# Performance work log

Hardware: AMD Instinct MI355X
Metric: run time of the kernel (lower is better)

The kernel has to match this reference:

```python
import jax, jax.numpy as jnp
import numpy as np

N_NODES = 100000
N_EDGES = 3200000
NFEAT, NHID, NCLASS = 512, 256, 64


def spmm(rows, cols, vals, x):
    # out[i] = sum_{e: rows[e]==i} vals[e] * x[cols[e]]
    msgs = vals[:, None] * x[cols]  # [E, F]
    return jax.ops.segment_sum(msgs, rows, num_segments=N_NODES)


def setup_inputs() -> dict:
    key = jax.random.key(0)
    ks = jax.random.split(key, 12)
    x = jax.random.normal(ks[0], (N_NODES, NFEAT), dtype=jnp.float32)
    adj_rows = jax.random.randint(ks[1], (N_EDGES,), 0, N_NODES, dtype=jnp.int32)
    adj_cols = jax.random.randint(ks[2], (N_EDGES,), 0, N_NODES, dtype=jnp.int32)
    adj_vals = jax.random.uniform(ks[3], (N_EDGES,), dtype=jnp.float32)
    # xavier-uniform style init for linear weights
    def xavier(k, fan_in, fan_out):
        a = np.sqrt(6.0 / (fan_in + fan_out)).astype(np.float32)
        return jax.random.uniform(k, (fan_in, fan_out), minval=-a, maxval=a, dtype=jnp.float32)
    W1 = xavier(ks[4], NFEAT, NHID)
    b1 = jnp.zeros((NHID,), dtype=jnp.float32)
    W2 = xavier(ks[5], NHID, NCLASS)
    b2 = jnp.zeros((NCLASS,), dtype=jnp.float32)
    Wres = xavier(ks[6], NHID, NCLASS)
    bres = jnp.zeros((NCLASS,), dtype=jnp.float32)
    return {"x": x, "adj_rows": adj_rows, "adj_cols": adj_cols, "adj_vals": adj_vals,
            "W1": W1, "b1": b1, "W2": W2, "b2": b2, "Wres": Wres, "bres": bres}


def reference(x, adj_rows, adj_cols, adj_vals, W1, b1, W2, b2, Wres, bres):
    # layer 1: spmm -> linear (res_con True but last_hidden is None -> no residual)
    h = spmm(adj_rows, adj_cols, adj_vals, x)          # [N, NFEAT]
    h = h @ W1 + b1                                    # [N, NHID]
    last_hidden = h
    # dropout in eval mode: identity
    # layer 2: spmm -> linear -> relu + res(last_hidden) since NHID != NCLASS
    o = spmm(adj_rows, adj_cols, adj_vals, h)          # [N, NHID]
    o = o @ W2 + b2                                    # [N, NCLASS]
    o = jax.nn.relu(o) + (last_hidden @ Wres + bres)   # [N, NCLASS]
    return o
```

## Files before the change

kernel.cpp:

```cpp
#include <hip/hip_runtime.h>

#define N_NODES 100000
#define N_EDGES 3200000
#define NFEAT 512
#define NHID 256
#define NCLASS 64
#define FCAT 128

#define RPB 32
#define NB 3125
#define CHUNK 16384
#define NCH 196

#define ISC20 (1.0f / 1048576.0f)
#define ISC14 (1.0f / 16384.0f)
#define ISC10 (1.0f / 1024.0f)

typedef __attribute__((ext_vector_type(8))) short short8;
typedef __attribute__((ext_vector_type(4))) float f32x4;

static __device__ __forceinline__ unsigned short f2bf(float f) {
    unsigned u = __float_as_uint(f);
    unsigned r = (u + 0x7FFF + ((u >> 16) & 1)) >> 16;
    return (unsigned short)r;
}
static __device__ __forceinline__ short8 cvt8(float4 x, float4 y) {
    short8 r;
    r[0] = (short)f2bf(x.x); r[1] = (short)f2bf(x.y);
    r[2] = (short)f2bf(x.z); r[3] = (short)f2bf(x.w);
    r[4] = (short)f2bf(y.x); r[5] = (short)f2bf(y.y);
    r[6] = (short)f2bf(y.z); r[7] = (short)f2bf(y.w);
    return r;
}
__device__ __forceinline__ void gload_lds16(const unsigned short* g, unsigned short* l) {
    __builtin_amdgcn_global_load_lds(
        (const __attribute__((address_space(1))) unsigned int*)g,
        (__attribute__((address_space(3))) unsigned int*)l, 16, 0, 0);
}
static __device__ __forceinline__ int f2q10(float a) {
    return __float2int_rn(fminf(fmaxf(a, -15.98f), 15.98f) * 1024.f);
}

__global__ __launch_bounds__(256) void k_fusedA(const float* __restrict__ W1,
                                                const float* __restrict__ W2,
                                                const float* __restrict__ Wres,
                                                const float* __restrict__ b1,
                                                const float* __restrict__ bres,
                                                unsigned short* __restrict__ WT,
                                                float* __restrict__ c2,
                                                float* __restrict__ cr,
                                                const int* __restrict__ rows,
                                                int* __restrict__ HT) {
    __shared__ int h[NB];
    int tid = threadIdx.x;
    if (blockIdx.x < 256) {
        int k = blockIdx.x * 2 + (tid >> 7);
        int j = tid & 127;
        const float* wb = (j < NCLASS) ? W2 : Wres;
        int jj = j & (NCLASS - 1);
        const float* w1row = W1 + (size_t)k * NHID;
        float acc = 0.f;
        for (int m = 0; m < NHID; ++m)
            acc += w1row[m] * wb[(size_t)m * NCLASS + jj];
        WT[(size_t)j * NFEAT + k] = f2bf(acc);
        return;
    }
    if (blockIdx.x == 256) {
        if (tid < 128) {
            int j = tid;
            const float* wb = (j < NCLASS) ? W2 : Wres;
            int jj = j & (NCLASS - 1);
            float acc = 0.f;
            for (int m = 0; m < NHID; ++m)
                acc += b1[m] * wb[(size_t)m * NCLASS + jj];
            if (j < NCLASS) c2[jj] = acc;
            else            cr[jj] = acc + bres[jj];
        }
        return;
    }
    int c = blockIdx.x - 257;
    for (int i = tid; i < NB; i += 256) h[i] = 0;
    __syncthreads();
    int e0 = c * CHUNK;
    int eend = e0 + CHUNK; if (eend > N_EDGES) eend = N_EDGES;
    int i = e0 + tid;
    for (; i + 7 * 256 < eend; i += 8 * 256) {
        int r[8];
#pragma unroll
        for (int u = 0; u < 8; ++u) r[u] = rows[i + u * 256];
#pragma unroll
        for (int u = 0; u < 8; ++u) atomicAdd(&h[r[u] >> 5], 1);
    }
    for (; i < eend; i += 256)
        atomicAdd(&h[rows[i] >> 5], 1);
    __syncthreads();
    for (int k = tid; k < NB; k += 256)
        HT[(size_t)k * NCH + c] = h[k];
}

__global__ void k_scan_chunks(const int* __restrict__ HT, int* __restrict__ OFS,
                              int* __restrict__ T) {
    int b = blockIdx.x;
    int lane = threadIdx.x;
    const int* hb = HT + (size_t)b * NCH;
    int run = 0;
    for (int c0 = 0; c0 < NCH; c0 += 64) {
        int idx = c0 + lane;
        int v = (idx < NCH) ? hb[idx] : 0;
        int inc = v;
#pragma unroll
        for (int d = 1; d < 64; d <<= 1) {
            int t = __shfl_up(inc, d);
            if (lane >= d) inc += t;
        }
        if (idx < NCH) OFS[(size_t)idx * NB + b] = run + inc - v;
        run += __shfl(inc, 63);
    }
    if (lane == 0) T[b] = run;
}

__global__ void k_scan_base(const int* __restrict__ T, int* __restrict__ base) {
    int lane = threadIdx.x;
    int run = 0;
    for (int c0 = 0; c0 < NB; c0 += 64) {
        int idx = c0 + lane;
        int v = (idx < NB) ? T[idx] : 0;
        int inc = v;
#pragma unroll
        for (int d = 1; d < 64; d <<= 1) {
            int t = __shfl_up(inc, d);
            if (lane >= d) inc += t;
        }
        if (idx < NB) base[idx] = run + inc - v;
        run += __shfl(inc, 63);
    }
    if (lane == 0) base[NB] = run;
}

#define GBK 64
__global__ __launch_bounds__(256) void k_fusedB(const int* __restrict__ rows,
                                                const int* __restrict__ cols,
                                                const float* __restrict__ vals,
                                                const int* __restrict__ OFS,
                                                const int* __restrict__ base,
                                                unsigned* __restrict__ stage,
                                                const float* __restrict__ X,
                                                const unsigned short* __restrict__ WT,
                                                unsigned* __restrict__ A2) {
    __shared__ __align__(16) char smem[32768];
    int tid = threadIdx.x;

    if (blockIdx.x < NCH) {
        int* cur = (int*)smem;
        int c = blockIdx.x;
        for (int i = tid; i < NB; i += 256)
            cur[i] = base[i] + OFS[(size_t)c * NB + i];
        __syncthreads();
        int e0 = c * CHUNK;
        int eend = e0 + CHUNK; if (eend > N_EDGES) eend = N_EDGES;
        int i = e0 + tid;
        for (; i + 7 * 256 < eend; i += 8 * 256) {
            int r[8], cc[8]; float v[8];
#pragma unroll
            for (int u = 0; u < 8; ++u) r[u] = rows[i + u * 256];
#pragma unroll
            for (int u = 0; u < 8; ++u) cc[u] = cols[i + u * 256];
#pragma unroll
            for (int u = 0; u < 8; ++u) v[u] = vals[i + u * 256];
            int p[8];
#pragma unroll
            for (int u = 0; u < 8; ++u) p[u] = atomicAdd(&cur[r[u] >> 5], 1);
#pragma unroll
            for (int u = 0; u < 8; ++u) {
                unsigned v10 = min(1023u, (unsigned)__float2int_rn(v[u] * 1024.f));
                stage[p[u]] = (((unsigned)(r[u] & 31)) << 27) |
                              (((unsigned)cc[u]) << 10) | v10;
            }
        }
        for (; i < eend; i += 256) {
            int r = rows[i];
            int p = atomicAdd(&cur[r >> 5], 1);
            unsigned v10 = min(1023u, (unsigned)__float2int_rn(vals[i] * 1024.f));
            stage[p] = (((unsigned)(r & 31)) << 27) | (((unsigned)cols[i]) << 10) | v10;
        }
        return;
    }

    unsigned short* Bs = (unsigned short*)smem;
    int g = blockIdx.x - NCH;
    int lane = tid & 63, w = tid >> 6;
    int lr = lane & 15, ls = lane >> 4;
    int row = g * 64 + w * 16 + lr;
    if (row >= N_NODES) row = N_NODES - 1;
    const float* pA = X + (size_t)row * NFEAT;

#define STAGE(buf, k0)                                                         \
    {                                                                          \
        _Pragma("unroll")                                                      \
        for (int q = 0; q < 4; ++q) {                                          \
            int sidx = q * 256 + tid;                                          \
            int n = sidx >> 3, c8 = sidx & 7;                                  \
            const unsigned short* src =                                        \
                WT + (size_t)n * NFEAT + (k0) + ((c8 ^ (n & 7)) << 3);         \
            unsigned short* dst =                                              \
                Bs + (size_t)(buf) * FCAT * GBK + (size_t)(q * 256 + w * 64) * 8; \
            gload_lds16(src, dst);                                             \
        }                                                                      \
    }

    f32x4 acc[8] = {};
    STAGE(0, 0);
    __syncthreads();
    int cur = 0;

#pragma unroll
    for (int t = 0; t < 8; ++t) {
        const int k0 = t * GBK;
        float4 a00 = *(const float4*)(pA + k0 + ls * 8);
        float4 a01 = *(const float4*)(pA + k0 + ls * 8 + 4);
        float4 a10 = *(const float4*)(pA + k0 + 32 + ls * 8);
        float4 a11 = *(const float4*)(pA + k0 + 32 + ls * 8 + 4);
        if (t < 7) STAGE(cur ^ 1, k0 + GBK);

        short8 af0 = cvt8(a00, a01);
        short8 af1 = cvt8(a10, a11);
        const unsigned short* bb = Bs + (size_t)cur * FCAT * GBK;
#pragma unroll
        for (int nf = 0; nf < 8; ++nf) {
            int n = nf * 16 + lr;
            int p0 = ls ^ (n & 7);
            int p1 = (4 + ls) ^ (n & 7);
            short8 b0 = *(const short8*)(bb + (size_t)n * 64 + p0 * 8);
            short8 b1 = *(const short8*)(bb + (size_t)n * 64 + p1 * 8);
            acc[nf] = __builtin_amdgcn_mfma_f32_16x16x32_bf16(af0, b0, acc[nf], 0, 0, 0);
            acc[nf] = __builtin_amdgcn_mfma_f32_16x16x32_bf16(af1, b1, acc[nf], 0, 0, 0);
        }
        __syncthreads();
        cur ^= 1;
    }
#undef STAGE

#pragma unroll
    for (int j = 0; j < 4; ++j) {
        int gr = g * 64 + w * 16 + ls * 4 + j;
        if (gr < N_NODES) {
#pragma unroll
            for (int nf = 0; nf < 4; ++nf) {
                int il = f2q10(acc[nf][j]);
                int ih = f2q10(acc[nf + 4][j]);
                A2[(size_t)gr * 64 + nf * 16 + lr] =
                    ((unsigned)il & 0xffffu) | ((unsigned)ih << 16);
            }
        }
    }
}

__global__ __launch_bounds__(256) void k_spmm1(const unsigned* __restrict__ A2,
                                               const int* __restrict__ base,
                                               const unsigned* __restrict__ stage,
                                               unsigned short* __restrict__ S1a,
                                               float* __restrict__ S1r) {
    __shared__ int acc[RPB][FCAT];
    int b = blockIdx.x, tid = threadIdx.x;
    int wv = tid >> 6, lane = tid & 63;
    unsigned lane4 = (unsigned)lane << 2;
    int4* az = (int4*)&acc[0][0];
    for (int i = tid; i < RPB * FCAT / 4; i += 256) az[i] = make_int4(0, 0, 0, 0);
    __syncthreads();

    const char* A2b = (const char*)A2;

    int s = base[b], e = base[b + 1];
    int per = (e - s + 3) >> 2;
    int ws = s + wv * per;
    int we = ws + per; if (we > e) we = e;
    int t = ws;
    for (; t + 16 <= we; t += 16) {
        unsigned cv[16];
#pragma unroll
        for (int u = 0; u < 16; ++u) cv[u] = stage[t + u];
        unsigned p[16];
#pragma unroll
        for (int u = 0; u < 16; ++u)
            p[u] = *(const unsigned*)(A2b + (((cv[u] & 0x07FFFC00u) >> 2) | lane4));
#pragma unroll
        for (int u = 0; u < 16; ++u) {
            int v10 = (int)(cv[u] & 0x3FFu);
            int alo = (int)(short)(p[u] & 0xffffu);
            int ahi = (int)p[u] >> 16;
            int rl = (int)(cv[u] >> 27);
            atomicAdd(&acc[rl][lane],      __mul24(alo, v10));
            atomicAdd(&acc[rl][lane + 64], __mul24(ahi, v10));
        }
    }
    for (; t < we; ++t) {
        unsigned cv = stage[t];
        unsigned p = *(const unsigned*)(A2b + (((cv & 0x07FFFC00u) >> 2) | lane4));
        int v10 = (int)(cv & 0x3FFu);
        int alo = (int)(short)(p & 0xffffu);
        int ahi = (int)p >> 16;
        int rl = (int)(cv >> 27);
        atomicAdd(&acc[rl][lane],      __mul24(alo, v10));
        atomicAdd(&acc[rl][lane + 64], __mul24(ahi, v10));
    }
    __syncthreads();

#pragma unroll
    for (int rr = 0; rr < 8; ++rr) {
        int r = wv * 8 + rr;
        int node = b * RPB + r;
        int sf = (acc[r][lane] + 2048) >> 12;
        sf = max(-32760, min(32760, sf));
        S1a[(size_t)node * 64 + (lane & 31) * 2 + (lane >> 5)] = (unsigned short)sf;
        S1r[(size_t)node * 64 + lane] = (float)acc[r][lane + 64] * ISC20;
    }
}

__global__ __launch_bounds__(256) void k_spmm2_out(const unsigned* __restrict__ S1aP,
                                                   const float* __restrict__ S1r,
                                                   const int* __restrict__ base,
                                                   const unsigned* __restrict__ stage,
                                                   const float* __restrict__ c2,
                                                   const float* __restrict__ cr,
                                                   const float* __restrict__ b2,
                                                   float* __restrict__ out) {
    __shared__ int acc[RPB][NCLASS];
    __shared__ int rs[RPB];
    int b = blockIdx.x, tid = threadIdx.x;
    int wv = tid >> 6, lane = tid & 63;
    int h = lane >> 5, l5 = lane & 31;
    unsigned l54 = (unsigned)l5 << 2;
    int4* az = (int4*)&acc[0][0];
    for (int i = tid; i < RPB * NCLASS / 4; i += 256) az[i] = make_int4(0, 0, 0, 0);
    if (tid < RPB) rs[tid] = 0;
    __syncthreads();

    const char* Sb = (const char*)S1aP;

    int s = base[b], e = base[b + 1];
    int per = (e - s + 3) >> 2;
    int ws = s + wv * per;
    int we = ws + per; if (we > e) we = e;
    int t = ws;
    for (; t + 16 <= we; t += 16) {
        unsigned cv[8];
#pragma unroll
        for (int u = 0; u < 8; ++u) cv[u] = stage[t + u * 2 + h];
        unsigned p[8];
#pragma unroll
        for (int u = 0; u < 8; ++u)
            p[u] = *(const unsigned*)(Sb + (((cv[u] & 0x07FFFC00u) >> 3) | l54));
#pragma unroll
        for (int u = 0; u < 8; ++u) {
            int v10 = (int)(cv[u] & 0x3FFu);
            int slo = (int)(short)(p[u] & 0xffffu);
            int shi = (int)p[u] >> 16;
            int rl = (int)(cv[u] >> 27);
            atomicAdd(&acc[rl][l5],      (__mul24(slo, v10) + 8) >> 4);
            atomicAdd(&acc[rl][l5 + 32], (__mul24(shi, v10) + 8) >> 4);
            if (l5 == 0) atomicAdd(&rs[rl], v10);
        }
    }
    for (; t < we; t += 2) {
        int idx = t + h;
        bool act = idx < we;
        unsigned cv = stage[act ? idx : t];
        unsigned p = *(const unsigned*)(Sb + (((cv & 0x07FFFC00u) >> 3) | l54));
        int v10 = (int)(cv & 0x3FFu);
        int slo = (int)(short)(p & 0xffffu);
        int shi = (int)p >> 16;
        int rl = (int)(cv >> 27);
        if (act) {
            atomicAdd(&acc[rl][l5],      (__mul24(slo, v10) + 8) >> 4);
            atomicAdd(&acc[rl][l5 + 32], (__mul24(shi, v10) + 8) >> 4);
            if (l5 == 0) atomicAdd(&rs[rl], v10);
        }
    }
    __syncthreads();

#pragma unroll
    for (int rr = 0; rr < 8; ++rr) {
        int r = wv * 8 + rr;
        int node = b * RPB + r;
        float facc = (float)acc[r][lane] * ISC14;
        float rsum = (float)rs[r] * ISC10;
        float o = facc + rsum * c2[lane] + b2[lane];
        float res = S1r[(size_t)node * 64 + lane] + cr[lane];
        out[(size_t)node * 64 + lane] = fmaxf(o, 0.f) + res;
    }
}

extern "C" void kernel_launch(void* const* d_in, const int* in_sizes, int n_in,
                              void* d_out, int out_size, void* d_ws, size_t ws_size,
                              hipStream_t stream) {
    const float* x        = (const float*)d_in[0];
    const int*   adj_rows = (const int*)d_in[1];
    const int*   adj_cols = (const int*)d_in[2];
    const float* adj_vals = (const float*)d_in[3];
    const float* W1       = (const float*)d_in[4];
    const float* b1       = (const float*)d_in[5];
    const float* W2       = (const float*)d_in[6];
    const float* b2       = (const float*)d_in[7];
    const float* Wres     = (const float*)d_in[8];
    const float* bres     = (const float*)d_in[9];
    float* out = (float*)d_out;

    char* ws = (char*)d_ws;
    size_t off = 0;
    auto alloc = [&](size_t bytes) {
        size_t o = off;
        off += (bytes + 511) & ~511ULL;
        return o;
    };

    unsigned short* WT  = (unsigned short*)(ws + alloc((size_t)NFEAT * FCAT * 2));
    float* c2           = (float*)(ws + alloc(NCLASS * 4));
    float* cr           = (float*)(ws + alloc(NCLASS * 4));
    unsigned* stage     = (unsigned*)(ws + alloc((size_t)N_EDGES * 4));
    unsigned* A2        = (unsigned*)(ws + alloc((size_t)N_NODES * 64 * 4));
    unsigned* S1a       = (unsigned*)(ws + alloc((size_t)N_NODES * 32 * 4));
    char* s1r_region    = ws + alloc((size_t)N_NODES * 64 * 4);
    float* S1r          = (float*)s1r_region;
    int*   HT           = (int*)s1r_region;
    int*   OFS          = (int*)(s1r_region + (((size_t)NB * NCH * 4 + 511) & ~511ULL));
    int*   T            = (int*)(ws + alloc((size_t)NB * 4));
    int*   base         = (int*)(ws + alloc((size_t)(NB + 1) * 4));
    (void)ws_size; (void)in_sizes; (void)n_in; (void)out_size;

    k_fusedA<<<257 + NCH, 256, 0, stream>>>(W1, W2, Wres, b1, bres, WT, c2, cr,
                                            adj_rows, HT);

    k_scan_chunks<<<NB, 64, 0, stream>>>(HT, OFS, T);
    k_scan_base<<<1, 64, 0, stream>>>(T, base);

    k_fusedB<<<NCH + (N_NODES + 63) / 64, 256, 0, stream>>>(
        adj_rows, adj_cols, adj_vals, OFS, base, stage, x, WT, A2);

    k_spmm1<<<NB, 256, 0, stream>>>(A2, base, stage, (unsigned short*)S1a, S1r);

    k_spmm2_out<<<NB, 256, 0, stream>>>(S1a, S1r, base, stage, c2, cr, b2, out);
}
```

Before: 323.6 us.

## Quantize projected features to int8, halve partition chunk, split fused kernel

Projected layer-1 features (A2) are now quantized to 4-bit-fraction int8 (range ±7.94) instead of 10-bit-fraction int16. This halves the gather traffic in the first SpMM, which is the bandwidth-bound random access over edges. The edge partition chunk size is halved so twice as many blocks scatter into the staging buffer. The fused partition+GEMM kernel is split into two separate launches. The much coarser quantization risks accuracy loss and clipping of large activations, and the extra launch adds overhead.

```diff
diff --git a/kernel.cpp b/kernel.cpp
--- a/kernel.cpp
+++ b/kernel.cpp
@@ -9,10 +9,9 @@
 
 #define RPB 32
 #define NB 3125
-#define CHUNK 16384
-#define NCH 196
-
-#define ISC20 (1.0f / 1048576.0f)
+#define CHUNK 8192
+#define NCH 391
+
 #define ISC14 (1.0f / 16384.0f)
 #define ISC10 (1.0f / 1024.0f)
 
@@ -37,8 +36,8 @@
         (const __attribute__((address_space(1))) unsigned int*)g,
         (__attribute__((address_space(3))) unsigned int*)l, 16, 0, 0);
 }
-static __device__ __forceinline__ int f2q10(float a) {
-    return __float2int_rn(fminf(fmaxf(a, -15.98f), 15.98f) * 1024.f);
+static __device__ __forceinline__ int f2q4(float a) {
+    return __float2int_rn(fminf(fmaxf(a, -7.9375f), 7.9375f) * 16.f);
 }
 
 __global__ __launch_bounds__(256) void k_fusedA(const float* __restrict__ W1,
@@ -137,60 +136,56 @@
     if (lane == 0) base[NB] = run;
 }
 
+__global__ __launch_bounds__(256) void k_partition(const int* __restrict__ rows,
+                                                   const int* __restrict__ cols,
+                                                   const float* __restrict__ vals,
+                                                   const int* __restrict__ OFS,
+                                                   const int* __restrict__ base,
+                                                   unsigned* __restrict__ stage) {
+    __shared__ int cur[NB];
+    int c = blockIdx.x;
+    int tid = threadIdx.x;
+    for (int i = tid; i < NB; i += 256)
+        cur[i] = base[i] + OFS[(size_t)c * NB + i];
+    __syncthreads();
+    int e0 = c * CHUNK;
+    int eend = e0 + CHUNK; if (eend > N_EDGES) eend = N_EDGES;
+    int i = e0 + tid;
+    for (; i + 7 * 256 < eend; i += 8 * 256) {
+        int r[8], cc[8]; float v[8];
+#pragma unroll
+        for (int u = 0; u < 8; ++u) r[u] = rows[i + u * 256];
+#pragma unroll
+        for (int u = 0; u < 8; ++u) cc[u] = cols[i + u * 256];
+#pragma unroll
+        for (int u = 0; u < 8; ++u) v[u] = vals[i + u * 256];
+        int p[8];
+#pragma unroll
+        for (int u = 0; u < 8; ++u) p[u] = atomicAdd(&cur[r[u] >> 5], 1);
+#pragma unroll
+        for (int u = 0; u < 8; ++u) {
+            unsigned v10 = min(1023u, (unsigned)__float2int_rn(v[u] * 1024.f));
+            stage[p[u]] = (((unsigned)(r[u] & 31)) << 27) |
+                          (((unsigned)cc[u]) << 10) | v10;
+        }
+    }
+    for (; i < eend; i += 256) {
+        int r = rows[i];
+        int p = atomicAdd(&cur[r >> 5], 1);
+        unsigned v10 = min(1023u, (unsigned)__float2int_rn(vals[i] * 1024.f));
+        stage[p] = (((unsigned)(r & 31)) << 27) | (((unsigned)cols[i]) << 10) | v10;
+    }
+}
+
 #define GBK 64
-__global__ __launch_bounds__(256) void k_fusedB(const int* __restrict__ rows,
-                                                const int* __restrict__ cols,
-                                                const float* __restrict__ vals,
-                                                const int* __restrict__ OFS,
-                                                const int* __restrict__ base,
-                                                unsigned* __restrict__ stage,
-                                                const float* __restrict__ X,
+__global__ __launch_bounds__(256) void k_gemm_a(const float* __restrict__ X,
                                                 const unsigned short* __restrict__ WT,
-                                                unsigned* __restrict__ A2) {
-    __shared__ __align__(16) char smem[32768];
+                                                unsigned short* __restrict__ A2) {
+    __shared__ __align__(16) unsigned short Bs[2][FCAT * GBK];
     int tid = threadIdx.x;
-
-    if (blockIdx.x < NCH) {
-        int* cur = (int*)smem;
-        int c = blockIdx.x;
-        for (int i = tid; i < NB; i += 256)
-            cur[i] = base[i] + OFS[(size_t)c * NB + i];
-        __syncthreads();
-        int e0 = c * CHUNK;
-        int eend = e0 + CHUNK; if (eend > N_EDGES) eend = N_EDGES;
-        int i = e0 + tid;
-        for (; i + 7 * 256 < eend; i += 8 * 256) {
-            int r[8], cc[8]; float v[8];
-#pragma unroll
-            for (int u = 0; u < 8; ++u) r[u] = rows[i + u * 256];
-#pragma unroll
-            for (int u = 0; u < 8; ++u) cc[u] = cols[i + u * 256];
-#pragma unroll
-            for (int u = 0; u < 8; ++u) v[u] = vals[i + u * 256];
-            int p[8];
-#pragma unroll
-            for (int u = 0; u < 8; ++u) p[u] = atomicAdd(&cur[r[u] >> 5], 1);
-#pragma unroll
-            for (int u = 0; u < 8; ++u) {
-                unsigned v10 = min(1023u, (unsigned)__float2int_rn(v[u] * 1024.f));
-                stage[p[u]] = (((unsigned)(r[u] & 31)) << 27) |
-                              (((unsigned)cc[u]) << 10) | v10;
-            }
-        }
-        for (; i < eend; i += 256) {
-            int r = rows[i];
-            int p = atomicAdd(&cur[r >> 5], 1);
-            unsigned v10 = min(1023u, (unsigned)__float2int_rn(vals[i] * 1024.f));
-            stage[p] = (((unsigned)(r & 31)) << 27) | (((unsigned)cols[i]) << 10) | v10;
-        }
-        return;
-    }
-
-    unsigned short* Bs = (unsigned short*)smem;
-    int g = blockIdx.x - NCH;
     int lane = tid & 63, w = tid >> 6;
     int lr = lane & 15, ls = lane >> 4;
-    int row = g * 64 + w * 16 + lr;
+    int row = blockIdx.x * 64 + w * 16 + lr;
     if (row >= N_NODES) row = N_NODES - 1;
     const float* pA = X + (size_t)row * NFEAT;
 
@@ -202,8 +197,7 @@
             int n = sidx >> 3, c8 = sidx & 7;                                  \
             const unsigned short* src =                                        \
                 WT + (size_t)n * NFEAT + (k0) + ((c8 ^ (n & 7)) << 3);         \
-            unsigned short* dst =                                              \
-                Bs + (size_t)(buf) * FCAT * GBK + (size_t)(q * 256 + w * 64) * 8; \
+            unsigned short* dst = &Bs[buf][(size_t)(q * 256 + w * 64) * 8];    \
             gload_lds16(src, dst);                                             \
         }                                                                      \
     }
@@ -224,7 +218,7 @@
 
         short8 af0 = cvt8(a00, a01);
         short8 af1 = cvt8(a10, a11);
-        const unsigned short* bb = Bs + (size_t)cur * FCAT * GBK;
+        const unsigned short* bb = &Bs[cur][0];
 #pragma unroll
         for (int nf = 0; nf < 8; ++nf) {
             int n = nf * 16 + lr;
@@ -242,20 +236,20 @@
 
 #pragma unroll
     for (int j = 0; j < 4; ++j) {
-        int gr = g * 64 + w * 16 + ls * 4 + j;
+        int gr = blockIdx.x * 64 + w * 16 + ls * 4 + j;
         if (gr < N_NODES) {
 #pragma unroll
             for (int nf = 0; nf < 4; ++nf) {
-                int il = f2q10(acc[nf][j]);
-                int ih = f2q10(acc[nf + 4][j]);
+                int il = f2q4(acc[nf][j]);
+                int ih = f2q4(acc[nf + 4][j]);
                 A2[(size_t)gr * 64 + nf * 16 + lr] =
-                    ((unsigned)il & 0xffffu) | ((unsigned)ih << 16);
+                    (unsigned short)(((unsigned)il & 0xffu) | (((unsigned)ih & 0xffu) << 8));
             }
         }
     }
 }
 
-__global__ __launch_bounds__(256) void k_spmm1(const unsigned* __restrict__ A2,
+__global__ __launch_bounds__(256) void k_spmm1(const unsigned short* __restrict__ A2,
                                                const int* __restrict__ base,
                                                const unsigned* __restrict__ stage,
                                                unsigned short* __restrict__ S1a,
@@ -263,7 +257,7 @@
     __shared__ int acc[RPB][FCAT];
     int b = blockIdx.x, tid = threadIdx.x;
     int wv = tid >> 6, lane = tid & 63;
-    unsigned lane4 = (unsigned)lane << 2;
+    unsigned lane2 = (unsigned)lane << 1;
     int4* az = (int4*)&acc[0][0];
     for (int i = tid; i < RPB * FCAT / 4; i += 256) az[i] = make_int4(0, 0, 0, 0);
     __syncthreads();
@@ -279,15 +273,15 @@
         unsigned cv[16];
 #pragma unroll
         for (int u = 0; u < 16; ++u) cv[u] = stage[t + u];
-        unsigned p[16];
+        unsigned short p[16];
 #pragma unroll
         for (int u = 0; u < 16; ++u)
-            p[u] = *(const unsigned*)(A2b + (((cv[u] & 0x07FFFC00u) >> 2) | lane4));
+            p[u] = *(const unsigned short*)(A2b + (((cv[u] & 0x07FFFC00u) >> 3) | lane2));
 #pragma unroll
         for (int u = 0; u < 16; ++u) {
             int v10 = (int)(cv[u] & 0x3FFu);
-            int alo = (int)(short)(p[u] & 0xffffu);
-            int ahi = (int)p[u] >> 16;
+            int alo = (int)(signed char)(p[u] & 0xffu);
+            int ahi = (int)(signed char)(p[u] >> 8);
             int rl = (int)(cv[u] >> 27);
             atomicAdd(&acc[rl][lane],      __mul24(alo, v10));
             atomicAdd(&acc[rl][lane + 64], __mul24(ahi, v10));
@@ -295,10 +289,10 @@
     }
     for (; t < we; ++t) {
         unsigned cv = stage[t];
-        unsigned p = *(const unsigned*)(A2b + (((cv & 0x07FFFC00u) >> 2) | lane4));
+        unsigned short p = *(const unsigned short*)(A2b + (((cv & 0x07FFFC00u) >> 3) | lane2));
         int v10 = (int)(cv & 0x3FFu);
-        int alo = (int)(short)(p & 0xffffu);
-        int ahi = (int)p >> 16;
+        int alo = (int)(signed char)(p & 0xffu);
+        int ahi = (int)(signed char)(p >> 8);
         int rl = (int)(cv >> 27);
         atomicAdd(&acc[rl][lane],      __mul24(alo, v10));
         atomicAdd(&acc[rl][lane + 64], __mul24(ahi, v10));
@@ -309,10 +303,10 @@
     for (int rr = 0; rr < 8; ++rr) {
         int r = wv * 8 + rr;
         int node = b * RPB + r;
-        int sf = (acc[r][lane] + 2048) >> 12;
+        int sf = (acc[r][lane] + 32) >> 6;
         sf = max(-32760, min(32760, sf));
         S1a[(size_t)node * 64 + (lane & 31) * 2 + (lane >> 5)] = (unsigned short)sf;
-        S1r[(size_t)node * 64 + lane] = (float)acc[r][lane + 64] * ISC20;
+        S1r[(size_t)node * 64 + lane] = (float)acc[r][lane + 64] * ISC14;
     }
 }
 
@@ -417,7 +411,7 @@
     float* c2           = (float*)(ws + alloc(NCLASS * 4));
     float* cr           = (float*)(ws + alloc(NCLASS * 4));
     unsigned* stage     = (unsigned*)(ws + alloc((size_t)N_EDGES * 4));
-    unsigned* A2        = (unsigned*)(ws + alloc((size_t)N_NODES * 64 * 4));
+    unsigned short* A2  = (unsigned short*)(ws + alloc((size_t)N_NODES * 64 * 2));
     unsigned* S1a       = (unsigned*)(ws + alloc((size_t)N_NODES * 32 * 4));
     char* s1r_region    = ws + alloc((size_t)N_NODES * 64 * 4);
     float* S1r          = (float*)s1r_region;
@@ -433,8 +427,9 @@
     k_scan_chunks<<<NB, 64, 0, stream>>>(HT, OFS, T);
     k_scan_base<<<1, 64, 0, stream>>>(T, base);
 
-    k_fusedB<<<NCH + (N_NODES + 63) / 64, 256, 0, stream>>>(
-        adj_rows, adj_cols, adj_vals, OFS, base, stage, x, WT, A2);
+    k_partition<<<NCH, 256, 0, stream>>>(adj_rows, adj_cols, adj_vals, OFS, base, stage);
+
+    k_gemm_a<<<(N_NODES + 63) / 64, 256, 0, stream>>>(x, WT, A2);
 
     k_spmm1<<<NB, 256, 0, stream>>>(A2, base, stage, (unsigned short*)S1a, S1r);
 
```

Result: no change. 320.5 us (-1.0%).
